# Kernel tuning notes

Measured on AMD Instinct MI355X. Metric: run time of the kernel, lower is better.

## Reference

```python
import jax, jax.numpy as jnp
import numpy as np

N_NODES = 50000
N_EDGES = 800000
NFEAT = 128
NHID = 128
NCLASS = 10
N_GRAPHS = 256


def _segment_mean(vals, idx, num):
    # scatter-mean: sum then divide by count, count clamped to 1 (PyG 'mean' semantics)
    s = jax.ops.segment_sum(vals, idx, num_segments=num)
    c = jax.ops.segment_sum(jnp.ones((vals.shape[0], 1), vals.dtype), idx, num_segments=num)
    return s / jnp.maximum(c, 1.0)


def _graph_conv(x, src, dst, W_n, b_n, W_s):
    # gather x at source nodes, scatter-mean into destination nodes
    agg = _segment_mean(x[src], dst, x.shape[0])          # [N, C_in]
    return agg @ W_n.T + b_n + x @ W_s.T                  # [N, C_out]


def setup_inputs() -> dict:
    key = jax.random.key(0)
    ks = jax.random.split(key, 12)

    def lin_w(k, o, i):
        return (jax.random.uniform(k, (o, i), jnp.float32) * 2.0 - 1.0) / np.sqrt(i)

    x = jax.random.normal(ks[0], (N_NODES, NFEAT), jnp.float32)
    edge_index = jax.random.randint(ks[1], (2, N_EDGES), 0, N_NODES, dtype=jnp.int32)
    batch = jnp.sort(jax.random.randint(ks[2], (N_NODES,), 0, N_GRAPHS, dtype=jnp.int32))

    return {
        "x": x,
        "edge_index": edge_index,
        "batch": batch,
        "W1n": lin_w(ks[3], NHID, NFEAT), "b1": jnp.zeros((NHID,), jnp.float32), "W1s": lin_w(ks[4], NHID, NFEAT),
        "W2n": lin_w(ks[5], NHID, NHID), "b2": jnp.zeros((NHID,), jnp.float32), "W2s": lin_w(ks[6], NHID, NHID),
        "W3n": lin_w(ks[7], NHID, NHID), "b3": jnp.zeros((NHID,), jnp.float32), "W3s": lin_w(ks[8], NHID, NHID),
        "Wlin": lin_w(ks[9], NCLASS, NHID), "blin": jnp.zeros((NCLASS,), jnp.float32),
    }


def reference(x, edge_index, batch, W1n, b1, W1s, W2n, b2, W2s, W3n, b3, W3s, Wlin, blin):
    src, dst = edge_index[0], edge_index[1]
    h = jax.nn.relu(_graph_conv(x, src, dst, W1n, b1, W1s))
    h = jax.nn.relu(_graph_conv(h, src, dst, W2n, b2, W2s))
    h = jax.nn.relu(_graph_conv(h, src, dst, W3n, b3, W3s))
    g = _segment_mean(h, batch, N_GRAPHS)                 # global_mean_pool -> [G, NHID]
    # dropout is identity at inference
    logits = g @ Wlin.T + blin                            # [G, NCLASS]
    return jax.nn.log_softmax(logits, axis=1)
```

## Files before the change

### kernel.cpp

```cpp
#include <hip/hip_runtime.h>
#include <hip/hip_bf16.h>

#define NNODES 50000
#define NEDGES 800000
#define NFEAT 128
#define NHID 128
#define NCLASS 10
#define NGRAPHS 256

#define NB 391
#define HB 128

typedef __attribute__((ext_vector_type(8))) short short8;
typedef __attribute__((ext_vector_type(4))) short short4v;
typedef __attribute__((ext_vector_type(4))) float floatx4;

__device__ __forceinline__ float bf2f(unsigned short u) {
    union { unsigned i; float f; } c; c.i = ((unsigned)u) << 16; return c.f;
}
__device__ __forceinline__ unsigned short f2bf(float f) {
    union { float f; unsigned i; } c; c.f = f;
    unsigned x = c.i;
    unsigned r = (x + 0x7fffu + ((x >> 16) & 1u)) >> 16;
    return (unsigned short)r;
}
__device__ __forceinline__ float blo(unsigned v) { return bf2f((unsigned short)(v & 0xffffu)); }
__device__ __forceinline__ float bhi(unsigned v) { return bf2f((unsigned short)(v >> 16)); }

__device__ __forceinline__ void gload_lds16(const void* gsrc, void* ldst) {
    __builtin_amdgcn_global_load_lds(
        (const __attribute__((address_space(1))) void*)gsrc,
        (__attribute__((address_space(3))) void*)ldst, 16, 0, 0);
}

__global__ __launch_bounds__(256) void k_hist(const int* __restrict__ dst,
                                              int* __restrict__ hist) {
    __shared__ int lh[NB];
    int tid = threadIdx.x;
    for (int b = tid; b < NB; b += 256) lh[b] = 0;
    __syncthreads();
    for (int i = blockIdx.x * 256 + tid; i < NEDGES; i += HB * 256)
        atomicAdd(&lh[dst[i] >> 7], 1);
    __syncthreads();
    for (int b = tid; b < NB; b += 256) hist[b * HB + blockIdx.x] = lh[b];
}

__global__ __launch_bounds__(512) void k_scan2(const int* __restrict__ hist,
                                               int* __restrict__ base,
                                               int* __restrict__ boff,
                                               int* __restrict__ row_ptr,
                                               const int* __restrict__ batch,
                                               int* __restrict__ gstart) {
    __shared__ int tot[NB];
    int tid = threadIdx.x;
    int wid = tid >> 6, l = tid & 63;
    if (tid <= NGRAPHS) {
        int lo = 0, hi = NNODES;
        while (lo < hi) { int mid = (lo + hi) >> 1; if (batch[mid] < tid) lo = mid + 1; else hi = mid; }
        gstart[tid] = lo;
    }
    for (int q = wid; q < NB; q += 8) {
        int h0 = hist[q * HB + l];
        int h1 = hist[q * HB + 64 + l];
        int s0 = h0, s1 = h1;
        #pragma unroll
        for (int d = 1; d < 64; d <<= 1) {
            int y0 = __shfl_up(s0, d);
            int y1 = __shfl_up(s1, d);
            if (l >= d) { s0 += y0; s1 += y1; }
        }
        int t0 = __shfl(s0, 63);
        base[q * HB + l] = s0 - h0;
        base[q * HB + 64 + l] = s1 - h1 + t0;
        if (l == 63) tot[q] = t0 + s1;
    }
    __syncthreads();
    if (wid == 0) {
        int carry = 0;
        #pragma unroll
        for (int c = 0; c < (NB + 63) / 64; ++c) {
            int i = c * 64 + l;
            int v = (i < NB) ? tot[i] : 0;
            int s = v;
            #pragma unroll
            for (int d = 1; d < 64; d <<= 1) { int y = __shfl_up(s, d); if (l >= d) s += y; }
            if (i < NB) boff[i] = carry + s - v;
            carry += __shfl(s, 63);
        }
        if (l == 0) { boff[NB] = carry; row_ptr[NNODES] = carry; }
    }
}

__global__ __launch_bounds__(256) void k_scatter(const int* __restrict__ src,
                                                 const int* __restrict__ dst,
                                                 const int* __restrict__ base,
                                                 const int* __restrict__ boff,
                                                 unsigned* __restrict__ ebuf) {
    __shared__ int cur[NB];
    int tid = threadIdx.x;
    for (int b = tid; b < NB; b += 256) cur[b] = boff[b] + base[b * HB + blockIdx.x];
    __syncthreads();
    for (int i = blockIdx.x * 256 + tid; i < NEDGES; i += HB * 256) {
        int d = dst[i];
        int bin = d >> 7;
        int pos = atomicAdd(&cur[bin], 1);
        ebuf[pos] = (unsigned)src[i] | ((unsigned)(d & 127) << 16);
    }
}

__global__ __launch_bounds__(256) void k_bcsr(const unsigned* __restrict__ ebuf,
                                              const int* __restrict__ boff,
                                              int* __restrict__ row_ptr,
                                              int* __restrict__ esrc) {
    __shared__ int deg[128];
    __shared__ int curs[128];
    int tid = threadIdx.x;
    int b = blockIdx.x;
    int s = boff[b], e = boff[b + 1];
    if (tid < 128) deg[tid] = 0;
    __syncthreads();
    for (int i = s + tid; i < e; i += 256) atomicAdd(&deg[ebuf[i] >> 16], 1);
    __syncthreads();
    if (tid == 0) {
        int run = s;
        for (int i = 0; i < 128; ++i) { curs[i] = run; run += deg[i]; }
    }
    __syncthreads();
    if (tid < 128) {
        int node = b * 128 + tid;
        if (node < NNODES) row_ptr[node] = curs[tid];
    }
    __syncthreads();
    for (int i = s + tid; i < e; i += 256) {
        unsigned pk = ebuf[i];
        int pos = atomicAdd(&curs[pk >> 16], 1);
        esrc[pos] = (int)(pk & 0xffffu);
    }
}

__global__ void k_cvt(const float* __restrict__ x,
                      const float* __restrict__ w0, const float* __restrict__ w1,
                      const float* __restrict__ w2, const float* __restrict__ w3,
                      const float* __restrict__ w4, const float* __restrict__ w5,
                      unsigned short* __restrict__ xb, unsigned short* __restrict__ wb) {
    int gid = blockIdx.x * blockDim.x + threadIdx.x;
    const int NX4 = NNODES * NFEAT / 4;
    const floatx4* srcv;
    short4v* dstv;
    if (gid < NX4) {
        srcv = (const floatx4*)x + gid;
        dstv = (short4v*)xb + gid;
    } else {
        int j = gid - NX4;
        if (j >= 6 * 4096) return;
        int m = j >> 12;
        int o4 = j & 4095;
        const float* w = (m == 0) ? w0 : (m == 1) ? w1 : (m == 2) ? w2
                       : (m == 3) ? w3 : (m == 4) ? w4 : w5;
        srcv = (const floatx4*)w + o4;
        dstv = (short4v*)wb + (m * 4096 + o4);
    }
    floatx4 v = *srcv;
    short4v o;
    #pragma unroll
    for (int k = 0; k < 4; ++k) o[k] = (short)f2bf(v[k]);
    *dstv = o;
}

__global__ __launch_bounds__(512, 6) void k_layer(const unsigned short* __restrict__ feat,
                                                  const int* __restrict__ row_ptr,
                                                  const int* __restrict__ esrc,
                                                  const unsigned short* __restrict__ Bn,
                                                  const unsigned short* __restrict__ Bs,
                                                  const float* __restrict__ bias,
                                                  unsigned short* __restrict__ out) {
    __shared__ __align__(16) unsigned short ldsA[2][8192];
    int w = threadIdx.x >> 6;
    int l = threadIdx.x & 63;
    int r = l & 15;
    int gk = l >> 4;
    int m0 = blockIdx.x * 64;

    {
        int c = l & 15;
        #pragma unroll
        for (int is = 0; is < 2; ++is) {
            int row = is * 32 + (w << 2) + (l >> 4);
            int nrow = m0 + row; if (nrow >= NNODES) nrow = NNODES - 1;
            gload_lds16(feat + (size_t)nrow * 128 + ((c ^ (row & 15)) << 3),
                        &ldsA[1][(is * 32 + (w << 2)) * 128]);
        }
    }

    const unsigned* feat32 = (const unsigned*)feat;
    unsigned* A1 = (unsigned*)&ldsA[0][0];
    #pragma unroll 1
    for (int i = 0; i < 8; ++i) {
        int row = (w << 3) + i;
        int n = m0 + row;
        float a0 = 0.f, a1 = 0.f;
        int nb = 0;
        if (n < NNODES) {
            int beg = row_ptr[n];
            nb = row_ptr[n + 1] - beg;
            for (int base = 0; base < nb; base += 64) {
                int rem = nb - base;
                int cnt = rem < 64 ? rem : 64;
                int myidx = (l < cnt) ? esrc[beg + base + l] : 0;
                int j = 0;
                for (; j + 8 <= cnt; j += 8) {
                    int s0 = __shfl(myidx, j);
                    int s1 = __shfl(myidx, j + 1);
                    int s2 = __shfl(myidx, j + 2);
                    int s3 = __shfl(myidx, j + 3);
                    int s4 = __shfl(myidx, j + 4);
                    int s5 = __shfl(myidx, j + 5);
                    int s6 = __shfl(myidx, j + 6);
                    int s7 = __shfl(myidx, j + 7);
                    unsigned v0 = feat32[s0 * 64 + l];
                    unsigned v1 = feat32[s1 * 64 + l];
                    unsigned v2 = feat32[s2 * 64 + l];
                    unsigned v3 = feat32[s3 * 64 + l];
                    unsigned v4 = feat32[s4 * 64 + l];
                    unsigned v5 = feat32[s5 * 64 + l];
                    unsigned v6 = feat32[s6 * 64 + l];
                    unsigned v7 = feat32[s7 * 64 + l];
                    a0 += ((blo(v0) + blo(v1)) + (blo(v2) + blo(v3)))
                        + ((blo(v4) + blo(v5)) + (blo(v6) + blo(v7)));
                    a1 += ((bhi(v0) + bhi(v1)) + (bhi(v2) + bhi(v3)))
                        + ((bhi(v4) + bhi(v5)) + (bhi(v6) + bhi(v7)));
                }
                for (; j + 4 <= cnt; j += 4) {
                    int s0 = __shfl(myidx, j);
                    int s1 = __shfl(myidx, j + 1);
                    int s2 = __shfl(myidx, j + 2);
                    int s3 = __shfl(myidx, j + 3);
                    unsigned v0 = feat32[s0 * 64 + l];
                    unsigned v1 = feat32[s1 * 64 + l];
                    unsigned v2 = feat32[s2 * 64 + l];
                    unsigned v3 = feat32[s3 * 64 + l];
                    a0 += (blo(v0) + blo(v1)) + (blo(v2) + blo(v3));
                    a1 += (bhi(v0) + bhi(v1)) + (bhi(v2) + bhi(v3));
                }
                for (; j < cnt; ++j) {
                    int s0 = __shfl(myidx, j);
                    unsigned v0 = feat32[s0 * 64 + l];
                    a0 += blo(v0);
                    a1 += bhi(v0);
                }
            }
        }
        float inv = 1.0f / (float)max(nb, 1);
        unsigned o = ((unsigned)f2bf(a0 * inv)) | (((unsigned)f2bf(a1 * inv)) << 16);
        int c = l >> 2;
        A1[row * 64 + ((c ^ (row & 15)) << 2) + (l & 3)] = o;
    }

    short8 bf[8];
    #pragma unroll
    for (int kt = 0; kt < 8; ++kt) {
        const unsigned short* Bbase = (kt < 4 ? Bn : Bs);
        bf[kt] = *(const short8*)(Bbase + (w * 16 + r) * 128 + (kt & 3) * 32 + gk * 8);
    }
    int o = w * 16 + r;
    float bias_v = bias[o];

    __syncthreads();

    #pragma unroll
    for (int t = 0; t < 4; ++t) {
        floatx4 acc = {0.f, 0.f, 0.f, 0.f};
        #pragma unroll
        for (int half = 0; half < 2; ++half) {
            short8 af[4];
            #pragma unroll
            for (int kk = 0; kk < 4; ++kk) {
                int Cr = (((kk << 2) + gk) ^ r) << 3;
                af[kk] = *(const short8*)(&ldsA[half][(t * 16 + r) * 128 + Cr]);
            }
            #pragma unroll
            for (int kk = 0; kk < 4; ++kk)
                acc = __builtin_amdgcn_mfma_f32_16x16x32_bf16(af[kk], bf[half * 4 + kk], acc, 0, 0, 0);
        }
        #pragma unroll
        for (int j = 0; j < 4; ++j) {
            int mrow = m0 + t * 16 + gk * 4 + j;
            if (mrow < NNODES) {
                float v = acc[j] + bias_v;
                v = v > 0.f ? v : 0.f;
                out[mrow * 128 + o] = f2bf(v);
            }
        }
    }
}

__global__ __launch_bounds__(256) void k_pool(const unsigned short* __restrict__ h,
                                              const int* __restrict__ gstart,
                                              float* __restrict__ part) {
    int g = blockIdx.x >> 3;
    int c = blockIdx.x & 7;
    int s = gstart[g], e = gstart[g + 1];
    int len = e - s;
    int cs = s + (len * c) / 8;
    int ce = s + (len * (c + 1)) / 8;
    int w = threadIdx.x >> 6;
    int l = threadIdx.x & 63;
    const unsigned* h32 = (const unsigned*)h;
    float a0 = 0.f, a1 = 0.f;
    for (int n = cs + w; n < ce; n += 4) {
        unsigned v = h32[n * 64 + l];
        a0 += blo(v);
        a1 += bhi(v);
    }
    __shared__ float red[4][128];
    red[w][2 * l] = a0;
    red[w][2 * l + 1] = a1;
    __syncthreads();
    if (w == 0) {
        float r0 = (red[0][2 * l] + red[1][2 * l]) + (red[2][2 * l] + red[3][2 * l]);
        float r1 = (red[0][2 * l + 1] + red[1][2 * l + 1]) + (red[2][2 * l + 1] + red[3][2 * l + 1]);
        float* dst = part + (size_t)(g * 8 + c) * 128;
        dst[2 * l] = r0;
        dst[2 * l + 1] = r1;
    }
}

__global__ __launch_bounds__(128) void k_head(const float* __restrict__ part,
                                              const int* __restrict__ gstart,
                                              const float* __restrict__ Wlin,
                                              const float* __restrict__ blin,
                                              float* __restrict__ out) {
    int gi = blockIdx.x;
    __shared__ float gl[128];
    __shared__ float lg[NCLASS];
    int t = threadIdx.x;
    float s = 0.f;
    #pragma unroll
    for (int c = 0; c < 8; ++c) s += part[(size_t)(gi * 8 + c) * 128 + t];
    int len = gstart[gi + 1] - gstart[gi];
    gl[t] = s / (float)max(len, 1);
    __syncthreads();
    if (t < NCLASS) {
        float a = blin[t];
        #pragma unroll 16
        for (int i = 0; i < 128; ++i) a += gl[i] * Wlin[t * 128 + i];
        lg[t] = a;
    }
    __syncthreads();
    if (t == 0) {
        float m = lg[0];
        for (int k = 1; k < NCLASS; ++k) m = fmaxf(m, lg[k]);
        float sum = 0.f;
        for (int k = 0; k < NCLASS; ++k) sum += expf(lg[k] - m);
        float ls = logf(sum) + m;
        for (int k = 0; k < NCLASS; ++k) out[gi * NCLASS + k] = lg[k] - ls;
    }
}

extern "C" void kernel_launch(void* const* d_in, const int* in_sizes, int n_in,
                              void* d_out, int out_size, void* d_ws, size_t ws_size,
                              hipStream_t stream) {
    const float* x    = (const float*)d_in[0];
    const int*   ei   = (const int*)d_in[1];
    const int*   src  = ei;
    const int*   dst  = ei + NEDGES;
    const int*   batch= (const int*)d_in[2];
    const float* W1n  = (const float*)d_in[3];
    const float* b1   = (const float*)d_in[4];
    const float* W1s  = (const float*)d_in[5];
    const float* W2n  = (const float*)d_in[6];
    const float* b2   = (const float*)d_in[7];
    const float* W2s  = (const float*)d_in[8];
    const float* W3n  = (const float*)d_in[9];
    const float* b3   = (const float*)d_in[10];
    const float* W3s  = (const float*)d_in[11];
    const float* Wlin = (const float*)d_in[12];
    const float* blin = (const float*)d_in[13];
    float* out = (float*)d_out;

    char* p = (char*)d_ws;
    auto alloc = [&](size_t bytes) -> void* {
        void* r = (void*)p;
        p += (bytes + 255) & ~(size_t)255;
        return r;
    };
    unsigned short* xb   = (unsigned short*)alloc((size_t)NNODES * NFEAT * 2);
    unsigned short* hA   = (unsigned short*)alloc((size_t)NNODES * NHID * 2);
    unsigned short* hB   = (unsigned short*)alloc((size_t)NNODES * NHID * 2);
    unsigned short* wb   = (unsigned short*)alloc((size_t)6 * 16384 * 2);
    int* hist    = (int*)alloc((size_t)NB * HB * 4);
    int* base    = (int*)alloc((size_t)NB * HB * 4);
    int* boff    = (int*)alloc((size_t)(NB + 1) * 4);
    int* row_ptr = (int*)alloc((size_t)(NNODES + 1) * 4);
    int* gstart  = (int*)alloc((size_t)(NGRAPHS + 1) * 4);
    unsigned* ebuf = (unsigned*)alloc((size_t)NEDGES * 4);
    int* esrc    = (int*)alloc((size_t)NEDGES * 4);
    float* part  = (float*)alloc((size_t)NGRAPHS * 8 * NHID * 4);

    k_hist<<<HB, 256, 0, stream>>>(dst, hist);
    k_scan2<<<1, 512, 0, stream>>>(hist, base, boff, row_ptr, batch, gstart);
    k_scatter<<<HB, 256, 0, stream>>>(src, dst, base, boff, ebuf);
    k_bcsr<<<NB, 256, 0, stream>>>(ebuf, boff, row_ptr, esrc);

    {
        int total4 = NNODES * NFEAT / 4 + 6 * 4096;
        k_cvt<<<(total4 + 255) / 256, 256, 0, stream>>>(x, W1n, W1s, W2n, W2s, W3n, W3s, xb, wb);
    }

    const int layerGrid = (NNODES + 63) / 64;

    k_layer<<<layerGrid, 512, 0, stream>>>(xb, row_ptr, esrc, wb + 0 * 16384, wb + 1 * 16384, b1, hA);
    k_layer<<<layerGrid, 512, 0, stream>>>(hA, row_ptr, esrc, wb + 2 * 16384, wb + 3 * 16384, b2, hB);
    k_layer<<<layerGrid, 512, 0, stream>>>(hB, row_ptr, esrc, wb + 4 * 16384, wb + 5 * 16384, b3, hA);

    k_pool<<<NGRAPHS * 8, 256, 0, stream>>>(hA, gstart, part);
    k_head<<<NGRAPHS, 128, 0, stream>>>(part, gstart, Wlin, blin, out);
}
```

Before: 205.0 us.

## Raise histogram block count and store CSR source indices as 16-bit

```diff
diff --git a/kernel.cpp b/kernel.cpp
--- a/kernel.cpp
+++ b/kernel.cpp
@@ -9,7 +9,7 @@
 #define NGRAPHS 256
 
 #define NB 391
-#define HB 128
+#define HB 512
 
 typedef __attribute__((ext_vector_type(8))) short short8;
 typedef __attribute__((ext_vector_type(4))) short short4v;
@@ -60,19 +60,17 @@
         gstart[tid] = lo;
     }
     for (int q = wid; q < NB; q += 8) {
-        int h0 = hist[q * HB + l];
-        int h1 = hist[q * HB + 64 + l];
-        int s0 = h0, s1 = h1;
+        int carry = 0;
         #pragma unroll
-        for (int d = 1; d < 64; d <<= 1) {
-            int y0 = __shfl_up(s0, d);
-            int y1 = __shfl_up(s1, d);
-            if (l >= d) { s0 += y0; s1 += y1; }
-        }
-        int t0 = __shfl(s0, 63);
-        base[q * HB + l] = s0 - h0;
-        base[q * HB + 64 + l] = s1 - h1 + t0;
-        if (l == 63) tot[q] = t0 + s1;
+        for (int c = 0; c < HB / 64; ++c) {
+            int h = hist[q * HB + c * 64 + l];
+            int s = h;
+            #pragma unroll
+            for (int d = 1; d < 64; d <<= 1) { int y = __shfl_up(s, d); if (l >= d) s += y; }
+            base[q * HB + c * 64 + l] = carry + s - h;
+            carry += __shfl(s, 63);
+        }
+        if (l == 0) tot[q] = carry;
     }
     __syncthreads();
     if (wid == 0) {
@@ -111,7 +109,7 @@
 __global__ __launch_bounds__(256) void k_bcsr(const unsigned* __restrict__ ebuf,
                                               const int* __restrict__ boff,
                                               int* __restrict__ row_ptr,
-                                              int* __restrict__ esrc) {
+                                              unsigned short* __restrict__ esrc) {
     __shared__ int deg[128];
     __shared__ int curs[128];
     int tid = threadIdx.x;
@@ -134,7 +132,7 @@
     for (int i = s + tid; i < e; i += 256) {
         unsigned pk = ebuf[i];
         int pos = atomicAdd(&curs[pk >> 16], 1);
-        esrc[pos] = (int)(pk & 0xffffu);
+        esrc[pos] = (unsigned short)(pk & 0xffffu);
     }
 }
 
@@ -169,7 +167,7 @@
 
 __global__ __launch_bounds__(512, 6) void k_layer(const unsigned short* __restrict__ feat,
                                                   const int* __restrict__ row_ptr,
-                                                  const int* __restrict__ esrc,
+                                                  const unsigned short* __restrict__ esrc,
                                                   const unsigned short* __restrict__ Bn,
                                                   const unsigned short* __restrict__ Bs,
                                                   const float* __restrict__ bias,
@@ -206,7 +204,7 @@
             for (int base = 0; base < nb; base += 64) {
                 int rem = nb - base;
                 int cnt = rem < 64 ? rem : 64;
-                int myidx = (l < cnt) ? esrc[beg + base + l] : 0;
+                int myidx = (l < cnt) ? (int)esrc[beg + base + l] : 0;
                 int j = 0;
                 for (; j + 8 <= cnt; j += 8) {
                     int s0 = __shfl(myidx, j);
@@ -394,7 +392,7 @@
     int* row_ptr = (int*)alloc((size_t)(NNODES + 1) * 4);
     int* gstart  = (int*)alloc((size_t)(NGRAPHS + 1) * 4);
     unsigned* ebuf = (unsigned*)alloc((size_t)NEDGES * 4);
-    int* esrc    = (int*)alloc((size_t)NEDGES * 4);
+    unsigned short* esrc = (unsigned short*)alloc((size_t)NEDGES * 2);
     float* part  = (float*)alloc((size_t)NGRAPHS * 8 * NHID * 4);
 
     k_hist<<<HB, 256, 0, stream>>>(dst, hist);
```

New measurement: 228.8 us. 1.12x slower.
